# Performance work log

Measured on AMD Instinct MI355X. Metric: run time of the kernel, lower is better.

## Reference

```python
import jax, jax.numpy as jnp
import numpy as np

NUM_TAGS = 19
START_ID = 17  # lbl_to_id['START_LBL']
PAD_ID = 18    # lbl_to_id['PAD_LBL']
NEG = -1000.0


def setup_inputs() -> dict:
    key = jax.random.key(0)
    k1, k2, k3 = jax.random.split(key, 3)
    B, L = 512, 2048
    P = jax.random.normal(k1, (B, L, NUM_TAGS), dtype=jnp.float32)
    T = jax.random.normal(k2, (NUM_TAGS, NUM_TAGS), dtype=jnp.float32)
    # contiguous-prefix valid mask, lengths in [1, L]
    lengths = jax.random.randint(k3, (B,), 1, L + 1)
    mask = jnp.arange(L)[None, :] < lengths[:, None]  # [B, L] bool
    return {"P": P, "T": T, "mask": mask}


def _viterbi_forward(P, T, mask):
    # P: [B, L, K] emissions; T[j, k] = score of transition prev=k -> cur=j
    B, L, K = P.shape
    DP0 = jnp.full((B, K), NEG, dtype=P.dtype).at[:, START_ID].set(0.0)

    def step(DP, xs):
        emit, m = xs  # emit: [B, K], m: [B] bool
        scores = DP[:, None, :] + T[None, :, :]        # [B, cur, prev]
        best = scores.max(axis=-1)                      # [B, K]
        arg = scores.argmax(axis=-1).astype(jnp.int32)  # [B, K] backpointers
        new_DP = best + emit
        DP = jnp.where(m[:, None], new_DP, DP)          # frozen past sequence end
        return DP, arg

    DP, choice = jax.lax.scan(
        step, DP0, (jnp.swapaxes(P, 0, 1), jnp.swapaxes(mask, 0, 1))
    )  # choice: [L, B, K]
    DP = DP + T[PAD_ID][None, :]  # transition into PAD at the end
    return DP, choice


def reference(P, T, mask):
    B, L, K = P.shape
    DP, choice = _viterbi_forward(P, T, mask)
    last = DP.argmax(axis=-1).astype(jnp.int32)          # [B] best final tag
    lengths = mask.sum(axis=-1).astype(jnp.int32)        # [B]
    bidx = jnp.arange(B)

    def back(c, t):
        # path[t] = choice[t+1][path[t+1]] for t < len-1; path[len-1] = last
        nxt = choice[jnp.minimum(t + 1, L - 1), bidx, c]  # [B]
        new_c = jnp.where(t < lengths - 1, nxt, c)
        out = jnp.where(t < lengths, new_c, -1)           # -1 pads beyond length
        return new_c, out

    _, outs = jax.lax.scan(back, last, jnp.arange(L - 1, -1, -1))  # [L, B]
    path = jnp.flip(jnp.swapaxes(outs, 0, 1), axis=1)  # [B, L], decoded tags
    return path
```

## Files before the change

kernel.cpp:

```cpp
#include <hip/hip_runtime.h>

#define Bn 512
#define Ln 2048
#define Kn 19
#define NEGV (-1000.0f)
#define START_IDn 17
#define PAD_IDn 18
#define SEG 64
#define PBYTES 79691776u


#define DP_CORE(BASE)                                                          \
    float4 q0 = *(const float4*)((BASE) + 0);                                  \
    float4 q1 = *(const float4*)((BASE) + 4);                                  \
    float4 q2 = *(const float4*)((BASE) + 8);                                  \
    float4 q3 = *(const float4*)((BASE) + 12);                                 \
    float4 q4 = *(const float4*)((BASE) + 16);            \
    float cand[Kn];                                                            \
    cand[0]  = q0.x + Trow[0];  cand[1]  = q0.y + Trow[1];                     \
    cand[2]  = q0.z + Trow[2];  cand[3]  = q0.w + Trow[3];                     \
    cand[4]  = q1.x + Trow[4];  cand[5]  = q1.y + Trow[5];                     \
    cand[6]  = q1.z + Trow[6];  cand[7]  = q1.w + Trow[7];                     \
    cand[8]  = q2.x + Trow[8];  cand[9]  = q2.y + Trow[9];                     \
    cand[10] = q2.z + Trow[10]; cand[11] = q2.w + Trow[11];                    \
    cand[12] = q3.x + Trow[12]; cand[13] = q3.y + Trow[13];                    \
    cand[14] = q3.z + Trow[14]; cand[15] = q3.w + Trow[15];                    \
    cand[16] = q4.x + Trow[16]; cand[17] = q4.y + Trow[17];                    \
    cand[18] = q4.z + Trow[18];                                                \
    float m0 = fmaxf(fmaxf(cand[0],  cand[1]),  cand[2]);                      \
    float m1 = fmaxf(fmaxf(cand[3],  cand[4]),  cand[5]);                      \
    float m2 = fmaxf(fmaxf(cand[6],  cand[7]),  cand[8]);                      \
    float m3 = fmaxf(fmaxf(cand[9],  cand[10]), cand[11]);                     \
    float m4 = fmaxf(fmaxf(cand[12], cand[13]), cand[14]);                     \
    float m5 = fmaxf(fmaxf(cand[15], cand[16]), cand[17]);                     \
    float n0 = fmaxf(fmaxf(m0, m1), m2);                                       \
    float n1 = fmaxf(fmaxf(m3, m4), cand[18]);                                 \
    float best = fmaxf(fmaxf(n0, n1), m5);

__global__ __launch_bounds__(192, 1) void crf_fused(
    const float* __restrict__ P, const float* __restrict__ T,
    const int* __restrict__ mask, float* __restrict__ dpfin,
    int* __restrict__ lens, unsigned char* __restrict__ choice)
{
    const int tid = threadIdx.x;
    const int w = tid >> 6;

    __shared__ float dp[2][32];
    __shared__ float ebuf[2][2][1280];
    __shared__ float ckbuf[2][32][20];
    __shared__ int   s_len2[2];
    __shared__ int   seg_done[2];
    __shared__ float rdp[2][2][32];
    __shared__ __align__(16) unsigned char rcbuf[2][2][1280];

    if (tid < 2) *(volatile int*)&seg_done[tid] = 0;
    __syncthreads();

    if (w == 0) {
        __builtin_amdgcn_s_setprio(1);
        const int lane = tid;
        const int half = lane >> 5;
        const int c = lane & 31;
        const int b = blockIdx.x * 2 + half;
        const int cc = (c < Kn) ? c : (Kn - 1);

        float Trow[Kn];
#pragma unroll
        for (int p = 0; p < Kn; ++p) Trow[p] = T[cc * Kn + p];

        const int* mrow = mask + (size_t)b * Ln;
        int sum = 0;
#pragma unroll
        for (int j = 0; j < Ln / 128; ++j) {
            int4 v = *(const int4*)(mrow + j * 128 + c * 4);
            sum += v.x + v.y + v.z + v.w;
        }
#pragma unroll
        for (int k = 1; k < 32; k <<= 1) sum += __shfl_xor(sum, k, 64);
        const int len = sum;
        if (c == 0) { lens[b] = len; s_len2[half] = len; }
        const int lenO = __shfl_xor(len, 32, 64);
        int maxlen = len > lenO ? len : lenO;
        int lmin = len < lenO ? len : lenO;
        lmin = __builtin_amdgcn_readfirstlane(lmin);
        int mlen = (maxlen + (SEG - 1)) & ~(SEG - 1);
        mlen = __builtin_amdgcn_readfirstlane(mlen);

        float mydp = (c == START_IDn) ? 0.0f : NEGV;
        dp[half][c] = mydp;

        const unsigned bbyte = (unsigned)b * (Ln * Kn * 4u);
        const unsigned limit = PBYTES - 16;
        const char* Pc = (const char*)P;
        float4 r[10];

#define STAGE_LOAD(ci)                                                         \
    { unsigned base_ = bbyte + (unsigned)(ci) * 4864u + ((unsigned)c << 4);    \
      _Pragma("unroll")                                                        \
      for (int i_ = 0; i_ < 10; ++i_) {                                        \
          unsigned o_ = base_ + (unsigned)i_ * 512u;                           \
          if (o_ > limit) o_ = limit;                                          \
          r[i_] = *(const float4*)(Pc + o_);                                   \
      } }
#define STAGE_WRITE(nb)                                                        \
    { float* d_ = &ebuf[nb][half][(unsigned)c << 2];                           \
      _Pragma("unroll")                                                        \
      for (int i_ = 0; i_ < 10; ++i_) *(float4*)(d_ + i_ * 128) = r[i_]; }

        int buf = 0;
        STAGE_LOAD(0);
        STAGE_WRITE(0);

        for (int t0 = 0; t0 < mlen; t0 += SEG) {
            if (c < Kn) ckbuf[half][t0 >> 6][c] = mydp;
            __threadfence_block();
            __asm__ __volatile__("" ::: "memory");
            if (c == 0) *(volatile int*)&seg_done[half] = (t0 >> 6) + 1;

            STAGE_LOAD((t0 >> 6) + 1);
            const float* ebl = &ebuf[buf][half][0];

            if (t0 + SEG <= lmin) {
                for (int tt = 0; tt < SEG; tt += 8) {
#pragma unroll
                    for (int u = 0; u < 8; ++u) {
                        const float e = ebl[(tt + u) * Kn + cc];
                        const float* base_ = &dp[half][0];
                        DP_CORE(base_)
                        mydp = best + e;
                        dp[half][c] = mydp;
                    }
                }
            } else {
                for (int tt = 0; tt < SEG; tt += 8) {
#pragma unroll
                    for (int u = 0; u < 8; ++u) {
                        const int t = t0 + tt + u;
                        const float e = ebl[(tt + u) * Kn + cc];
                        const float* base_ = &dp[half][0];
                        DP_CORE(base_)
                        float nd = best + e;
                        mydp = (t < len) ? nd : mydp;
                        dp[half][c] = mydp;
                    }
                }
            }
            STAGE_WRITE(buf ^ 1);
            buf ^= 1;
        }
        if (c < Kn) dpfin[b * Kn + c] = mydp;
        __threadfence_block();
        if (c == 0) *(volatile int*)&seg_done[half] = 32;
#undef STAGE_LOAD
#undef STAGE_WRITE
    } else {
        const int rw = w - 1;
        const int l = tid & 63;
        const int rhalf = l >> 5;
        const int rc = l & 31;
        const int cc = (rc < Kn) ? rc : (Kn - 1);
        const int b = blockIdx.x * 2 + rhalf;

        float Trow[Kn];
#pragma unroll
        for (int p = 0; p < Kn; ++p) Trow[p] = T[cc * Kn + p];

        const float* pbase = P + (size_t)b * Ln * Kn;
        int len = Ln + 1;

        for (int s = rw; s < 32; s += 2) {
            bool need = (s * SEG) < len;
            if (!__any(need)) break;
            while (true) {
                int f = *(volatile int*)&seg_done[rhalf];
                if (__all((!need) || (f >= s + 1))) break;
                __builtin_amdgcn_s_sleep(8);
            }
            __asm__ __volatile__("" ::: "memory");
            if (len > Ln) {
                len = *(volatile int*)&s_len2[rhalf];
                need = (s * SEG) < len;
            }
            if (need) {
                const int t0 = s * SEG;
                float mydp = (rc < Kn) ? ckbuf[rhalf][s][rc] : NEGV;
                rdp[rw][rhalf][rc] = mydp;
                const float* prow = pbase + (size_t)t0 * Kn;

                float eb[8];
#pragma unroll
                for (int u = 0; u < 8; ++u) eb[u] = prow[u * Kn + cc];

                for (int tt = 0; tt < SEG; tt += 8) {
#pragma unroll
                    for (int u = 0; u < 8; ++u) {
                        const int t = t0 + tt + u;
                        const float e = eb[u];
                        const float* base_ = &rdp[rw][rhalf][0];
                        DP_CORE(base_)
                        float nd = best + e;
                        mydp = (t < len) ? nd : mydp;
                        rdp[rw][rhalf][rc] = mydp;

                        int arg = Kn - 1;
#pragma unroll
                        for (int p = Kn - 2; p >= 0; --p)
                            arg = (cand[p] == best) ? p : arg;
                        if (rc < Kn)
                            rcbuf[rw][rhalf][(tt + u) * Kn + rc] = (unsigned char)arg;

                        int tn = tt + u + 8;
                        int tloc = (t0 + tn < Ln) ? tn : (Ln - 1 - t0);
                        eb[u] = prow[tloc * Kn + cc];
                    }
                }
                const int4* s4 = (const int4*)&rcbuf[rw][rhalf][0];
                int4* d4 = (int4*)(choice + (size_t)b * Ln * Kn + (size_t)t0 * Kn);
                for (int i = rc; i < (SEG * Kn) / 16; i += 32) d4[i] = s4[i];
            }
        }
    }
}

__global__ __launch_bounds__(384, 1) void crf_bwd(
    const float* __restrict__ T, const unsigned char* __restrict__ choice,
    const float* __restrict__ dpfin, const int* __restrict__ lens,
    int* __restrict__ out)
{
    __shared__ unsigned char comp[Ln * Kn];
    __shared__ int vchain[17];
    __shared__ int s_last, s_len;

    const int b = blockIdx.x;
    const int tid = threadIdx.x;

    {
        const int4* src = (const int4*)(choice + (size_t)b * Ln * Kn);
        int4* dst = (int4*)comp;
        for (int i = tid; i < (Ln * Kn) / 16; i += 384) dst[i] = src[i];
    }
    if (tid == 0) {
        s_len = lens[b];
        float bestv = dpfin[b * Kn + 0] + T[PAD_IDn * Kn + 0];
        int bl = 0;
        for (int ci = 1; ci < Kn; ++ci) {
            float v = dpfin[b * Kn + ci] + T[PAD_IDn * Kn + ci];
            if (v > bestv) { bestv = v; bl = ci; }
        }
        s_last = bl;
    }
    __syncthreads();
    const int len = s_len;

    {
        const int wv = tid >> 6;
        const int lane = tid & 63;
        const int ch = wv * 3 + lane / Kn;
        const int c = lane % Kn;
        if (lane < 3 * Kn && ch < 16) {
            int cur = c;
            const int tb = ch * 128 + 127;
            for (int i = 0; i < 128; ++i) {
                const int t = tb - i;
                int nv = comp[t * Kn + cur];
                cur = (t < len) ? nv : cur;
                comp[t * Kn + c] = cur;
            }
        }
    }
    __syncthreads();

    if (tid == 0) {
        int v = s_last;
        vchain[16] = v;
        for (int ch = 15; ch >= 0; --ch) {
            v = comp[ch * 128 * Kn + v];
            vchain[ch] = v;
        }
    }
    __syncthreads();

    const int last = s_last;
    int* orow = out + (size_t)b * Ln;
    for (int t = tid; t < Ln; t += 384) {
        int val;
        if (t >= len) {
            val = -1;
        } else if (t == Ln - 1) {
            val = last;
        } else {
            const int tp = t + 1;
            const int vc = vchain[(tp >> 7) + 1];
            val = comp[tp * Kn + vc];
        }
        orow[t] = val;
    }
}

extern "C" void kernel_launch(void* const* d_in, const int* in_sizes, int n_in,
                              void* d_out, int out_size, void* d_ws, size_t ws_size,
                              hipStream_t stream)
{
    const float* P    = (const float*)d_in[0];
    const float* T    = (const float*)d_in[1];
    const int*   mask = (const int*)d_in[2];
    int* out = (int*)d_out;

    const size_t choice_bytes = (size_t)Bn * Ln * Kn;
    unsigned char* choice = (unsigned char*)d_ws;
    float* dpfin = (float*)((char*)d_ws + choice_bytes);
    int* lens = (int*)((char*)d_ws + choice_bytes + (size_t)Bn * Kn * 4);

    crf_fused<<<Bn / 2, 192, 0, stream>>>(P, T, mask, dpfin, lens, choice);
    crf_bwd<<<Bn, 384, 0, stream>>>(T, choice, dpfin, lens, out);
}
```

Measured before the change: 411.2 us.

## Give each recompute wave one sequence and broadcast DP via readlane

The recompute (backpointer) warps change from two waves each handling two sequences in 32-lane halves to four waves, each owning one sequence and a segment parity. The DP vector moves from shared memory to registers: each step broadcasts the previous DP values with readlane instead of writing and reading LDS. This removes an LDS round trip from the serial dependency chain on every step and doubles the number of waves doing recompute. The cost is a larger block (320 threads) and lanes 19..63 of each wave doing no useful work.

```diff
diff --git a/kernel.cpp b/kernel.cpp
--- a/kernel.cpp
+++ b/kernel.cpp
@@ -27,6 +27,9 @@
     cand[14] = q3.z + Trow[14]; cand[15] = q3.w + Trow[15];                    \
     cand[16] = q4.x + Trow[16]; cand[17] = q4.y + Trow[17];                    \
     cand[18] = q4.z + Trow[18];                                                \
+    MAXTREE()
+
+#define MAXTREE()                                                              \
     float m0 = fmaxf(fmaxf(cand[0],  cand[1]),  cand[2]);                      \
     float m1 = fmaxf(fmaxf(cand[3],  cand[4]),  cand[5]);                      \
     float m2 = fmaxf(fmaxf(cand[6],  cand[7]),  cand[8]);                      \
@@ -37,7 +40,20 @@
     float n1 = fmaxf(fmaxf(m3, m4), cand[18]);                                 \
     float best = fmaxf(fmaxf(n0, n1), m5);
 
-__global__ __launch_bounds__(192, 1) void crf_fused(
+#define RL(p) (__uint_as_float((unsigned)__builtin_amdgcn_readlane(            \
+                   (int)__float_as_uint(mydp), (p))) + Trow[p])
+#define REC_CORE()                                                             \
+    float cand[Kn];                                                            \
+    cand[0]  = RL(0);  cand[1]  = RL(1);  cand[2]  = RL(2);                    \
+    cand[3]  = RL(3);  cand[4]  = RL(4);  cand[5]  = RL(5);                    \
+    cand[6]  = RL(6);  cand[7]  = RL(7);  cand[8]  = RL(8);                    \
+    cand[9]  = RL(9);  cand[10] = RL(10); cand[11] = RL(11);                   \
+    cand[12] = RL(12); cand[13] = RL(13); cand[14] = RL(14);                   \
+    cand[15] = RL(15); cand[16] = RL(16); cand[17] = RL(17);                   \
+    cand[18] = RL(18);                                                         \
+    MAXTREE()
+
+__global__ __launch_bounds__(320, 1) void crf_fused(
     const float* __restrict__ P, const float* __restrict__ T,
     const int* __restrict__ mask, float* __restrict__ dpfin,
     int* __restrict__ lens, unsigned char* __restrict__ choice)
@@ -50,8 +66,7 @@
     __shared__ float ckbuf[2][32][20];
     __shared__ int   s_len2[2];
     __shared__ int   seg_done[2];
-    __shared__ float rdp[2][2][32];
-    __shared__ __align__(16) unsigned char rcbuf[2][2][1280];
+    __shared__ __align__(16) unsigned char rcbuf[4][1280];
 
     if (tid < 2) *(volatile int*)&seg_done[tid] = 0;
     __syncthreads();
@@ -154,69 +169,60 @@
 #undef STAGE_LOAD
 #undef STAGE_WRITE
     } else {
-        const int rw = w - 1;
-        const int l = tid & 63;
-        const int rhalf = l >> 5;
-        const int rc = l & 31;
-        const int cc = (rc < Kn) ? rc : (Kn - 1);
-        const int b = blockIdx.x * 2 + rhalf;
+        const int e = w - 1;
+        const int h = e & 1;
+        const int par = e >> 1;
+        const int lane = tid & 63;
+        const int cc = (lane < Kn) ? lane : (Kn - 1);
+        const int b = blockIdx.x * 2 + h;
 
         float Trow[Kn];
 #pragma unroll
         for (int p = 0; p < Kn; ++p) Trow[p] = T[cc * Kn + p];
 
         const float* pbase = P + (size_t)b * Ln * Kn;
-        int len = Ln + 1;
-
-        for (int s = rw; s < 32; s += 2) {
-            bool need = (s * SEG) < len;
-            if (!__any(need)) break;
-            while (true) {
-                int f = *(volatile int*)&seg_done[rhalf];
-                if (__all((!need) || (f >= s + 1))) break;
-                __builtin_amdgcn_s_sleep(8);
+        volatile int* vf = &seg_done[h];
+
+        while (*vf < 1) __builtin_amdgcn_s_sleep(8);
+        __asm__ __volatile__("" ::: "memory");
+        const int len = s_len2[h];
+
+        for (int s = par; s * SEG < len; s += 2) {
+            while (*vf < s + 1) __builtin_amdgcn_s_sleep(8);
+            __asm__ __volatile__("" ::: "memory");
+
+            const int t0 = s * SEG;
+            float mydp = (lane < Kn) ? ckbuf[h][s][lane] : NEGV;
+            const float* prow = pbase + (size_t)t0 * Kn;
+
+            float eb[8];
+#pragma unroll
+            for (int u = 0; u < 8; ++u) eb[u] = prow[u * Kn + cc];
+
+            for (int tt = 0; tt < SEG; tt += 8) {
+#pragma unroll
+                for (int u = 0; u < 8; ++u) {
+                    const int t = t0 + tt + u;
+                    REC_CORE()
+                    float nd = best + eb[u];
+                    mydp = (t < len) ? nd : mydp;
+
+                    int arg = Kn - 1;
+#pragma unroll
+                    for (int p = Kn - 2; p >= 0; --p)
+                        arg = (cand[p] == best) ? p : arg;
+                    if (lane < Kn)
+                        rcbuf[e][(tt + u) * Kn + lane] = (unsigned char)arg;
+
+                    int tn = tt + u + 8;
+                    int tloc = (t0 + tn < Ln) ? tn : (Ln - 1 - t0);
+                    eb[u] = prow[tloc * Kn + cc];
+                }
             }
-            __asm__ __volatile__("" ::: "memory");
-            if (len > Ln) {
-                len = *(volatile int*)&s_len2[rhalf];
-                need = (s * SEG) < len;
-            }
-            if (need) {
-                const int t0 = s * SEG;
-                float mydp = (rc < Kn) ? ckbuf[rhalf][s][rc] : NEGV;
-                rdp[rw][rhalf][rc] = mydp;
-                const float* prow = pbase + (size_t)t0 * Kn;
-
-                float eb[8];
-#pragma unroll
-                for (int u = 0; u < 8; ++u) eb[u] = prow[u * Kn + cc];
-
-                for (int tt = 0; tt < SEG; tt += 8) {
-#pragma unroll
-                    for (int u = 0; u < 8; ++u) {
-                        const int t = t0 + tt + u;
-                        const float e = eb[u];
-                        const float* base_ = &rdp[rw][rhalf][0];
-                        DP_CORE(base_)
-                        float nd = best + e;
-                        mydp = (t < len) ? nd : mydp;
-                        rdp[rw][rhalf][rc] = mydp;
-
-                        int arg = Kn - 1;
-#pragma unroll
-                        for (int p = Kn - 2; p >= 0; --p)
-                            arg = (cand[p] == best) ? p : arg;
-                        if (rc < Kn)
-                            rcbuf[rw][rhalf][(tt + u) * Kn + rc] = (unsigned char)arg;
-
-                        int tn = tt + u + 8;
-                        int tloc = (t0 + tn < Ln) ? tn : (Ln - 1 - t0);
-                        eb[u] = prow[tloc * Kn + cc];
-                    }
-                }
-                const int4* s4 = (const int4*)&rcbuf[rw][rhalf][0];
+            {
+                const int4* s4 = (const int4*)&rcbuf[e][0];
                 int4* d4 = (int4*)(choice + (size_t)b * Ln * Kn + (size_t)t0 * Kn);
-                for (int i = rc; i < (SEG * Kn) / 16; i += 32) d4[i] = s4[i];
+                for (int i = lane; i < (SEG * Kn) / 16; i += 64) d4[i] = s4[i];
             }
         }
     }
@@ -311,6 +317,6 @@
     float* dpfin = (float*)((char*)d_ws + choice_bytes);
     int* lens = (int*)((char*)d_ws + choice_bytes + (size_t)Bn * Kn * 4);
 
-    crf_fused<<<Bn / 2, 192, 0, stream>>>(P, T, mask, dpfin, lens, choice);
+    crf_fused<<<Bn / 2, 320, 0, stream>>>(P, T, mask, dpfin, lens, choice);
     crf_bwd<<<Bn, 384, 0, stream>>>(T, choice, dpfin, lens, out);
 }
```

New measurement: 448.4 us. 9.0% more time.

## Replace spin-wait flags with barrier-synchronized wavefront schedule between forward and recompute waves

Applied to the files above, without the earlier changes.

Removes the shared-memory seg_done flag polling with s_sleep and instead runs a lockstep schedule of 17 phases separated by __syncthreads. In each phase the forward wave computes two segments while the two recompute waves process the segments checkpointed in the previous phase. The recompute lane mapping also changes to 21 lanes per sequence, with per-lane active predicates. This adds a block barrier per phase, so a recompute wave that finishes early now waits for the forward wave, and it may couple the critical forward path to recompute progress.

```diff
diff --git a/kernel.cpp b/kernel.cpp
--- a/kernel.cpp
+++ b/kernel.cpp
@@ -43,59 +43,42 @@
     int* __restrict__ lens, unsigned char* __restrict__ choice)
 {
     const int tid = threadIdx.x;
-    const int w = tid >> 6;
-
-    __shared__ float dp[2][32];
+    const int wv = tid >> 6;
+    const int lane = tid & 63;
+
+    __shared__ float dpf[2][32];
     __shared__ float ebuf[2][2][1280];
     __shared__ float ckbuf[2][32][20];
-    __shared__ int   s_len2[2];
-    __shared__ int   seg_done[2];
-    __shared__ float rdp[2][2][32];
+    __shared__ float dpr[2][2][20];
     __shared__ __align__(16) unsigned char rcbuf[2][2][1280];
-
-    if (tid < 2) *(volatile int*)&seg_done[tid] = 0;
-    __syncthreads();
-
-    if (w == 0) {
-        __builtin_amdgcn_s_setprio(1);
-        const int lane = tid;
-        const int half = lane >> 5;
-        const int c = lane & 31;
-        const int b = blockIdx.x * 2 + half;
-        const int cc = (c < Kn) ? c : (Kn - 1);
-
-        float Trow[Kn];
-#pragma unroll
-        for (int p = 0; p < Kn; ++p) Trow[p] = T[cc * Kn + p];
-
-        const int* mrow = mask + (size_t)b * Ln;
-        int sum = 0;
-#pragma unroll
-        for (int j = 0; j < Ln / 128; ++j) {
-            int4 v = *(const int4*)(mrow + j * 128 + c * 4);
-            sum += v.x + v.y + v.z + v.w;
-        }
-#pragma unroll
-        for (int k = 1; k < 32; k <<= 1) sum += __shfl_xor(sum, k, 64);
-        const int len = sum;
-        if (c == 0) { lens[b] = len; s_len2[half] = len; }
-        const int lenO = __shfl_xor(len, 32, 64);
-        int maxlen = len > lenO ? len : lenO;
-        int lmin = len < lenO ? len : lenO;
-        lmin = __builtin_amdgcn_readfirstlane(lmin);
-        int mlen = (maxlen + (SEG - 1)) & ~(SEG - 1);
-        mlen = __builtin_amdgcn_readfirstlane(mlen);
-
-        float mydp = (c == START_IDn) ? 0.0f : NEGV;
-        dp[half][c] = mydp;
-
-        const unsigned bbyte = (unsigned)b * (Ln * Kn * 4u);
-        const unsigned limit = PBYTES - 16;
-        const char* Pc = (const char*)P;
-        float4 r[10];
+    __shared__ int s_len2[2];
+
+    const int half = lane >> 5;
+    const int cF = lane & 31;
+    const int bF = blockIdx.x * 2 + half;
+    const int ccF = (cF < Kn) ? cF : (Kn - 1);
+    int lmin = 0, mlen = 0, buf = 0, lenF = 0;
+    float mydpF = NEGV;
+    const unsigned bbyte = (unsigned)bF * (Ln * Kn * 4u);
+    const unsigned limit = PBYTES - 16;
+    const char* Pc = (const char*)P;
+    float4 r[10];
+
+    const int rw = wv - 1;
+    const int g = lane / 21;
+    const int cR = lane - g * 21;
+    const bool gv = (g < 2);
+    const int h = gv ? g : 1;
+    const int bR = blockIdx.x * 2 + h;
+    const int ccR = (cR < Kn) ? cR : (Kn - 1);
+
+    const int cidx = (wv == 0) ? ccF : ccR;
+    float Trow[Kn];
+#pragma unroll
+    for (int p = 0; p < Kn; ++p) Trow[p] = T[cidx * Kn + p];
 
 #define STAGE_LOAD(ci)                                                         \
-    { unsigned base_ = bbyte + (unsigned)(ci) * 4864u + ((unsigned)c << 4);    \
+    { unsigned base_ = bbyte + (unsigned)(ci) * 4864u + ((unsigned)cF << 4);   \
       _Pragma("unroll")                                                        \
       for (int i_ = 0; i_ < 10; ++i_) {                                        \
           unsigned o_ = base_ + (unsigned)i_ * 512u;                           \
@@ -103,123 +86,132 @@
           r[i_] = *(const float4*)(Pc + o_);                                   \
       } }
 #define STAGE_WRITE(nb)                                                        \
-    { float* d_ = &ebuf[nb][half][(unsigned)c << 2];                           \
+    { float* d_ = &ebuf[nb][half][(unsigned)cF << 2];                          \
       _Pragma("unroll")                                                        \
       for (int i_ = 0; i_ < 10; ++i_) *(float4*)(d_ + i_ * 128) = r[i_]; }
 
-        int buf = 0;
+    if (wv == 0) {
+        __builtin_amdgcn_s_setprio(1);
+        const int* mrow = mask + (size_t)bF * Ln;
+        int sum = 0;
+#pragma unroll
+        for (int j = 0; j < Ln / 128; ++j) {
+            int4 v = *(const int4*)(mrow + j * 128 + cF * 4);
+            sum += v.x + v.y + v.z + v.w;
+        }
+#pragma unroll
+        for (int k = 1; k < 32; k <<= 1) sum += __shfl_xor(sum, k, 64);
+        lenF = sum;
+        if (cF == 0) { lens[bF] = lenF; s_len2[half] = lenF; }
+        const int lenO = __shfl_xor(lenF, 32, 64);
+        int maxlen = lenF > lenO ? lenF : lenO;
+        int lm = lenF < lenO ? lenF : lenO;
+        lmin = __builtin_amdgcn_readfirstlane(lm);
+        int ml = (maxlen + (SEG - 1)) & ~(SEG - 1);
+        mlen = __builtin_amdgcn_readfirstlane(ml);
+
+        mydpF = (cF == START_IDn) ? 0.0f : NEGV;
+        dpf[half][cF] = mydpF;
+
         STAGE_LOAD(0);
         STAGE_WRITE(0);
-
-        for (int t0 = 0; t0 < mlen; t0 += SEG) {
-            if (c < Kn) ckbuf[half][t0 >> 6][c] = mydp;
-            __threadfence_block();
-            __asm__ __volatile__("" ::: "memory");
-            if (c == 0) *(volatile int*)&seg_done[half] = (t0 >> 6) + 1;
-
-            STAGE_LOAD((t0 >> 6) + 1);
-            const float* ebl = &ebuf[buf][half][0];
-
-            if (t0 + SEG <= lmin) {
-                for (int tt = 0; tt < SEG; tt += 8) {
-#pragma unroll
-                    for (int u = 0; u < 8; ++u) {
-                        const float e = ebl[(tt + u) * Kn + cc];
-                        const float* base_ = &dp[half][0];
-                        DP_CORE(base_)
-                        mydp = best + e;
-                        dp[half][c] = mydp;
-                    }
-                }
-            } else {
-                for (int tt = 0; tt < SEG; tt += 8) {
-#pragma unroll
-                    for (int u = 0; u < 8; ++u) {
-                        const int t = t0 + tt + u;
-                        const float e = ebl[(tt + u) * Kn + cc];
-                        const float* base_ = &dp[half][0];
-                        DP_CORE(base_)
-                        float nd = best + e;
-                        mydp = (t < len) ? nd : mydp;
-                        dp[half][c] = mydp;
+    }
+    __syncthreads();
+
+    const int len0 = s_len2[0], len1 = s_len2[1];
+    const int lenR = (h == 0) ? len0 : len1;
+    const int lenmax = (len0 > len1) ? len0 : len1;
+
+    for (int w = 0; w < 17; ++w) {
+        if (wv == 0) {
+            if (w < 16) {
+#pragma unroll 1
+                for (int s2 = 0; s2 < 2; ++s2) {
+                    const int sg = 2 * w + s2;
+                    const int t0 = sg * SEG;
+                    if (t0 < mlen) {
+                        if (cF < Kn) ckbuf[half][sg][cF] = mydpF;
+                        STAGE_LOAD(sg + 1);
+                        const float* ebl = &ebuf[buf][half][0];
+
+                        if (t0 + SEG <= lmin) {
+                            for (int tt = 0; tt < SEG; tt += 8) {
+#pragma unroll
+                                for (int u = 0; u < 8; ++u) {
+                                    const float e = ebl[(tt + u) * Kn + ccF];
+                                    const float* base_ = &dpf[half][0];
+                                    DP_CORE(base_)
+                                    mydpF = best + e;
+                                    dpf[half][cF] = mydpF;
+                                }
+                            }
+                        } else {
+                            for (int tt = 0; tt < SEG; tt += 8) {
+#pragma unroll
+                                for (int u = 0; u < 8; ++u) {
+                                    const int t = t0 + tt + u;
+                                    const float e = ebl[(tt + u) * Kn + ccF];
+                                    const float* base_ = &dpf[half][0];
+                                    DP_CORE(base_)
+                                    float nd = best + e;
+                                    mydpF = (t < lenF) ? nd : mydpF;
+                                    dpf[half][cF] = mydpF;
+                                }
+                            }
+                        }
+                        STAGE_WRITE(buf ^ 1);
+                        buf ^= 1;
                     }
                 }
             }
-            STAGE_WRITE(buf ^ 1);
-            buf ^= 1;
-        }
-        if (c < Kn) dpfin[b * Kn + c] = mydp;
-        __threadfence_block();
-        if (c == 0) *(volatile int*)&seg_done[half] = 32;
-#undef STAGE_LOAD
-#undef STAGE_WRITE
-    } else {
-        const int rw = w - 1;
-        const int l = tid & 63;
-        const int rhalf = l >> 5;
-        const int rc = l & 31;
-        const int cc = (rc < Kn) ? rc : (Kn - 1);
-        const int b = blockIdx.x * 2 + rhalf;
-
-        float Trow[Kn];
-#pragma unroll
-        for (int p = 0; p < Kn; ++p) Trow[p] = T[cc * Kn + p];
-
-        const float* pbase = P + (size_t)b * Ln * Kn;
-        int len = Ln + 1;
-
-        for (int s = rw; s < 32; s += 2) {
-            bool need = (s * SEG) < len;
-            if (!__any(need)) break;
-            while (true) {
-                int f = *(volatile int*)&seg_done[rhalf];
-                if (__all((!need) || (f >= s + 1))) break;
-                __builtin_amdgcn_s_sleep(8);
-            }
-            __asm__ __volatile__("" ::: "memory");
-            if (len > Ln) {
-                len = *(volatile int*)&s_len2[rhalf];
-                need = (s * SEG) < len;
-            }
-            if (need) {
-                const int t0 = s * SEG;
-                float mydp = (rc < Kn) ? ckbuf[rhalf][s][rc] : NEGV;
-                rdp[rw][rhalf][rc] = mydp;
-                const float* prow = pbase + (size_t)t0 * Kn;
+        } else if (w >= 1) {
+            const int sg = 2 * (w - 1) + rw;
+            const int t0 = sg * SEG;
+            if (t0 < lenmax) {
+                const bool active = gv && (t0 < lenR);
+                float mydp = (active && cR < Kn) ? ckbuf[h][sg][cR] : NEGV;
+                if (active && cR < Kn) dpr[rw][h][cR] = mydp;
+                const float* prow = P + (size_t)bR * Ln * Kn + (size_t)t0 * Kn;
 
                 float eb[8];
 #pragma unroll
-                for (int u = 0; u < 8; ++u) eb[u] = prow[u * Kn + cc];
+                for (int u = 0; u < 8; ++u) eb[u] = prow[u * Kn + ccR];
 
                 for (int tt = 0; tt < SEG; tt += 8) {
 #pragma unroll
                     for (int u = 0; u < 8; ++u) {
                         const int t = t0 + tt + u;
                         const float e = eb[u];
-                        const float* base_ = &rdp[rw][rhalf][0];
+                        const float* base_ = &dpr[rw][h][0];
                         DP_CORE(base_)
                         float nd = best + e;
-                        mydp = (t < len) ? nd : mydp;
-                        rdp[rw][rhalf][rc] = mydp;
+                        mydp = (t < lenR) ? nd : mydp;
+                        if (active && cR < Kn) dpr[rw][h][cR] = mydp;
 
                         int arg = Kn - 1;
 #pragma unroll
                         for (int p = Kn - 2; p >= 0; --p)
                             arg = (cand[p] == best) ? p : arg;
-                        if (rc < Kn)
-                            rcbuf[rw][rhalf][(tt + u) * Kn + rc] = (unsigned char)arg;
+                        if (active && cR < Kn)
+                            rcbuf[rw][h][(tt + u) * Kn + cR] = (unsigned char)arg;
 
                         int tn = tt + u + 8;
                         int tloc = (t0 + tn < Ln) ? tn : (Ln - 1 - t0);
-                        eb[u] = prow[tloc * Kn + cc];
+                        eb[u] = prow[tloc * Kn + ccR];
                     }
                 }
-                const int4* s4 = (const int4*)&rcbuf[rw][rhalf][0];
-                int4* d4 = (int4*)(choice + (size_t)b * Ln * Kn + (size_t)t0 * Kn);
-                for (int i = rc; i < (SEG * Kn) / 16; i += 32) d4[i] = s4[i];
+                if (active) {
+                    const int4* s4 = (const int4*)&rcbuf[rw][h][0];
+                    int4* d4 = (int4*)(choice + (size_t)bR * Ln * Kn + (size_t)t0 * Kn);
+                    for (int i = cR; i < (SEG * Kn) / 16; i += 21) d4[i] = s4[i];
+                }
             }
         }
-    }
+        __syncthreads();
+    }
+    if (wv == 0 && cF < Kn) dpfin[bF * Kn + cF] = mydpF;
+#undef STAGE_LOAD
+#undef STAGE_WRITE
 }
 
 __global__ __launch_bounds__(384, 1) void crf_bwd(
```

Measured after the change: 416.3 us. No clear change (+1.2%).
